# Optimization experiments

Measured on AMD Instinct MI355X. Metric: run time of the kernel, lower is better.

Reference implementation:

```python
import jax, jax.numpy as jnp
import numpy as np

B, N, D, H = 256, 256, 136, 128  # queries, docs/query, feature dim, hidden dim


def setup_inputs() -> dict:
    key = jax.random.key(0)
    ks = jax.random.split(key, 7)
    features = jax.random.uniform(ks[0], (B, N, D), dtype=jnp.float32)
    labels = jax.random.randint(ks[1], (B, N), 0, 5, dtype=jnp.int32)  # relevance grades 0..4
    # Small init scales keep MLP scores in (-1, 1) so log2(1 + max(s_i, s_j)) is well-defined
    W1 = jax.random.normal(ks[2], (D, H), dtype=jnp.float32) * 0.05
    b1 = jnp.zeros((H,), dtype=jnp.float32)
    W2 = jax.random.normal(ks[3], (H, H), dtype=jnp.float32) * 0.05
    b2 = jnp.zeros((H,), dtype=jnp.float32)
    W3 = jax.random.normal(ks[4], (H, 1), dtype=jnp.float32) * 0.02
    b3 = jnp.zeros((1,), dtype=jnp.float32)
    return {"features": features, "labels": labels,
            "W1": W1, "b1": b1, "W2": W2, "b2": b2, "W3": W3, "b3": b3}


def _scores(features, W1, b1, W2, b2, W3, b3):
    # Linear-ReLU-(Dropout: identity in eval)-Linear-ReLU-Linear, then squeeze(-1)
    h = jax.nn.relu(jnp.einsum('bnd,dh->bnh', features, W1) + b1)
    h = jax.nn.relu(jnp.einsum('bnh,hk->bnk', h, W2) + b2)
    return (jnp.einsum('bnh,ho->bno', h, W3) + b3).squeeze(-1)  # [B, N]


def _compute_lambdas(scores, labels):
    si = scores[:, :, None]        # s_i  [B, N, 1]
    sj = scores[:, None, :]        # s_j  [B, 1, N]
    li = labels[:, :, None]
    lj = labels[:, None, :]
    # lambda_ij = 0.5 * (1 - sigmoid(s_j - s_i)) = 0.5 * sigmoid(s_i - s_j)
    lam = 0.5 * jax.nn.sigmoid(si - sj)
    gain = jnp.exp2(labels.astype(scores.dtype))  # 2 ** l
    dndcg = jnp.abs((gain[:, :, None] - gain[:, None, :])
                    / (1.0 + jnp.log2(1.0 + jnp.maximum(si, sj))))
    A = jnp.where(li > lj, lam * dndcg, jnp.zeros((), scores.dtype))  # [B, N, N]
    # lambdas[i] += A[i, j] over j (pairs where l_i > l_j); lambdas[j] -= A[i, j]
    return A.sum(-1) - A.sum(-2)  # [B, N]


def reference(features, labels, W1, b1, W2, b2, W3, b3):
    scores = _scores(features, W1, b1, W2, b2, W3, b3)
    return _compute_lambdas(scores, labels)
```

## Files before the change

kernel.cpp:

```cpp
#include <hip/hip_runtime.h>
#include <hip/hip_bf16.h>

#define DIN  136
#define HH   128
#define NSEQ 256
#define NB   256
#define BROWS 64
#define K1P  168
#define JB   8

typedef __attribute__((ext_vector_type(4))) float f32x4;
typedef __attribute__((ext_vector_type(2))) float f32x2;
typedef __attribute__((ext_vector_type(8))) short bf16x8;

static __device__ __forceinline__ unsigned short f2bf(float f) {
    unsigned int u = __float_as_uint(f);
    u += 0x7fffu + ((u >> 16) & 1u);
    return (unsigned short)(u >> 16);
}

__global__ __launch_bounds__(256)
void prep_kernel(const float* __restrict__ W1, const float* __restrict__ W2,
                 short* __restrict__ w1t, short* __restrict__ w2t)
{
    const int nt = gridDim.x * 256;
    const int idx = blockIdx.x * 256 + threadIdx.x;
    for (int e = idx; e < HH * K1P; e += nt) {
        const int n = e / K1P, k = e - n * K1P;
        w1t[e] = (k < DIN) ? (short)f2bf(W1[k * HH + n]) : (short)0;
    }
    for (int e = idx; e < HH * HH; e += nt) {
        const int n = e >> 7, k = e & 127;
        w2t[e] = (short)f2bf(W2[k * HH + n]);
    }
}

__global__ __launch_bounds__(256)
void scores_mfma_kernel(const float* __restrict__ features,
                        const int*   __restrict__ labels,
                        const short* __restrict__ w1t,
                        const short* __restrict__ w2t,
                        const float* __restrict__ b1, const float* __restrict__ b2,
                        const float* __restrict__ W3, const float* __restrict__ b3,
                        float4* __restrict__ pack,
                        float* __restrict__ out_zero)
{
    __shared__ short a_lds[BROWS * K1P];

    const int t    = threadIdx.x;
    const int lane = t & 63;
    const int wv   = t >> 6;
    const int l15  = lane & 15;
    const int l4   = lane >> 4;
    const long row0 = (long)blockIdx.x * BROWS;

    {
        const f32x2* src = (const f32x2*)(features + row0 * DIN);
        for (int i = t; i < BROWS * DIN / 2; i += 256) {
            f32x2 v = src[i];
            const int e = i * 2;
            const int r = e / DIN, k = e - r * DIN;
            *(unsigned int*)&a_lds[r * K1P + k] =
                (unsigned int)f2bf(v.x) | ((unsigned int)f2bf(v.y) << 16);
        }
        for (int i = t; i < BROWS * 16; i += 256) {
            const int r = i >> 4, k = DIN + (i & 15) * 2;
            *(unsigned int*)&a_lds[r * K1P + k] = 0u;
        }
    }
    __syncthreads();

    const int arow = (wv * 16 + l15) * K1P;

    f32x4 acc[8];
#pragma unroll
    for (int tn = 0; tn < 8; ++tn) {
        const float bv = b1[tn * 16 + l15];
        acc[tn] = (f32x4){bv, bv, bv, bv};
    }
    for (int kc = 0; kc < 5; ++kc) {
        const int kb = kc * 32 + l4 * 8;
        const bf16x8 afr = *(const bf16x8*)&a_lds[arow + kb];
        bf16x8 bfr[8];
#pragma unroll
        for (int tn = 0; tn < 8; ++tn)
            bfr[tn] = *(const bf16x8*)&w1t[(tn * 16 + l15) * K1P + kb];
#pragma unroll
        for (int tn = 0; tn < 8; ++tn)
            acc[tn] = __builtin_amdgcn_mfma_f32_16x16x32_bf16(afr, bfr[tn], acc[tn], 0, 0, 0);
    }
    __syncthreads();

#pragma unroll
    for (int tn = 0; tn < 8; ++tn) {
        const int col = tn * 16 + l15;
#pragma unroll
        for (int j = 0; j < 4; ++j)
            a_lds[(wv * 16 + l4 * 4 + j) * K1P + col] =
                (short)f2bf(fmaxf(acc[tn][j], 0.f));
    }
    __syncthreads();

    f32x4 acc2[8];
#pragma unroll
    for (int tn = 0; tn < 8; ++tn) {
        const float bv = b2[tn * 16 + l15];
        acc2[tn] = (f32x4){bv, bv, bv, bv};
    }
    for (int kc = 0; kc < 4; ++kc) {
        const int kb = kc * 32 + l4 * 8;
        const bf16x8 afr = *(const bf16x8*)&a_lds[arow + kb];
        bf16x8 bfr[8];
#pragma unroll
        for (int tn = 0; tn < 8; ++tn)
            bfr[tn] = *(const bf16x8*)&w2t[(tn * 16 + l15) * HH + kb];
#pragma unroll
        for (int tn = 0; tn < 8; ++tn)
            acc2[tn] = __builtin_amdgcn_mfma_f32_16x16x32_bf16(afr, bfr[tn], acc2[tn], 0, 0, 0);
    }

    {
        float w3v[8];
#pragma unroll
        for (int tn = 0; tn < 8; ++tn) w3v[tn] = W3[tn * 16 + l15];
        const float b3v = b3[0];
#pragma unroll
        for (int j = 0; j < 4; ++j) {
            float p = 0.f;
#pragma unroll
            for (int tn = 0; tn < 8; ++tn)
                p += fmaxf(acc2[tn][j], 0.f) * w3v[tn];
            p += __shfl_xor(p, 1, 64);
            p += __shfl_xor(p, 2, 64);
            p += __shfl_xor(p, 4, 64);
            p += __shfl_xor(p, 8, 64);
            if (l15 == 0) {
                const int row = wv * 16 + l4 * 4 + j;
                const long gr = row0 + row;
                const float s = p + b3v;
                const int lab = labels[gr];
                const float g = 0.5f * exp2f((float)lab);
                const float disc = 1.f / (1.f + log2f(1.f + s));
                pack[gr] = make_float4(s * 1.44269504088896f,
                                       g, disc, 0.f);
                out_zero[gr] = 0.f;
            }
        }
    }
}

__global__ __launch_bounds__(256)
void lambda_pair_kernel(const float4* __restrict__ pack,
                        float* __restrict__ out)
{
    __shared__ float4 sp[NSEQ];
    const int t  = threadIdx.x;
    const int b  = blockIdx.x >> 3;
    const int jo = (blockIdx.x & 7) * (NSEQ / JB);

    const float4 me = pack[b * NSEQ + t];
    sp[t] = me;
    __syncthreads();

    const float sci = me.x, gi = me.y, di = me.z;
    float accum = 0.f;
#pragma unroll 8
    for (int jj = 0; jj < NSEQ / JB; ++jj) {
        const float4 o = sp[jo + jj];
        const float dg = o.y - gi;
        const float e  = exp2f(o.x - sci);
        const float r  = __builtin_amdgcn_rcpf(1.f + e);
        const float dmax = (sci > o.x) ? di : o.z;
        const float dn = fabsf(dg) * dmax;
        const float w  = (dg < 0.f) ? r : (r - 1.f);
        accum += dn * w;
    }
    atomicAdd(&out[b * NSEQ + t], accum);
}

extern "C" void kernel_launch(void* const* d_in, const int* in_sizes, int n_in,
                              void* d_out, int out_size, void* d_ws, size_t ws_size,
                              hipStream_t stream)
{
    const float* features = (const float*)d_in[0];
    const int*   labels   = (const int*)d_in[1];
    const float* W1 = (const float*)d_in[2];
    const float* b1 = (const float*)d_in[3];
    const float* W2 = (const float*)d_in[4];
    const float* b2 = (const float*)d_in[5];
    const float* W3 = (const float*)d_in[6];
    const float* b3 = (const float*)d_in[7];

    float4* pack = (float4*)d_ws;
    short*  w1t  = (short*)((char*)d_ws + (size_t)NB * NSEQ * 16);
    short*  w2t  = w1t + HH * K1P;
    float*  out  = (float*)d_out;

    prep_kernel<<<64, 256, 0, stream>>>(W1, W2, w1t, w2t);
    scores_mfma_kernel<<<NB * NSEQ / BROWS, 256, 0, stream>>>(
        features, labels, w1t, w2t, b1, b2, W3, b3, pack, out);
    lambda_pair_kernel<<<NB * JB, 256, 0, stream>>>(pack, out);
}
```

Measured before the change: 124.4 us.

## Fuse score MLP and pairwise lambda kernels into one per-query block

New measurement: 121.8 us. 1.02x faster.

```diff
diff --git a/kernel.cpp b/kernel.cpp
--- a/kernel.cpp
+++ b/kernel.cpp
@@ -5,9 +5,7 @@
 #define HH   128
 #define NSEQ 256
 #define NB   256
-#define BROWS 64
 #define K1P  168
-#define JB   8
 
 typedef __attribute__((ext_vector_type(4))) float f32x4;
 typedef __attribute__((ext_vector_type(2))) float f32x2;
@@ -35,35 +33,36 @@
     }
 }
 
-__global__ __launch_bounds__(256)
-void scores_mfma_kernel(const float* __restrict__ features,
-                        const int*   __restrict__ labels,
-                        const short* __restrict__ w1t,
-                        const short* __restrict__ w2t,
-                        const float* __restrict__ b1, const float* __restrict__ b2,
-                        const float* __restrict__ W3, const float* __restrict__ b3,
-                        float4* __restrict__ pack,
-                        float* __restrict__ out_zero)
+__global__ __launch_bounds__(1024, 4)
+void fused_kernel(const float* __restrict__ features,
+                  const int*   __restrict__ labels,
+                  const short* __restrict__ w1t,
+                  const short* __restrict__ w2t,
+                  const float* __restrict__ b1, const float* __restrict__ b2,
+                  const float* __restrict__ W3, const float* __restrict__ b3,
+                  float* __restrict__ out)
 {
-    __shared__ short a_lds[BROWS * K1P];
+    __shared__ short  a_lds[NSEQ * K1P];
+    __shared__ float4 sp[NSEQ];
+    __shared__ float  s_part[4][NSEQ];
 
     const int t    = threadIdx.x;
     const int lane = t & 63;
     const int wv   = t >> 6;
     const int l15  = lane & 15;
     const int l4   = lane >> 4;
-    const long row0 = (long)blockIdx.x * BROWS;
+    const long row0 = (long)blockIdx.x * NSEQ;
 
     {
         const f32x2* src = (const f32x2*)(features + row0 * DIN);
-        for (int i = t; i < BROWS * DIN / 2; i += 256) {
+        for (int i = t; i < NSEQ * DIN / 2; i += 1024) {
             f32x2 v = src[i];
             const int e = i * 2;
             const int r = e / DIN, k = e - r * DIN;
             *(unsigned int*)&a_lds[r * K1P + k] =
                 (unsigned int)f2bf(v.x) | ((unsigned int)f2bf(v.y) << 16);
         }
-        for (int i = t; i < BROWS * 16; i += 256) {
+        for (int i = t; i < NSEQ * 16; i += 1024) {
             const int r = i >> 4, k = DIN + (i & 15) * 2;
             *(unsigned int*)&a_lds[r * K1P + k] = 0u;
         }
@@ -89,7 +88,6 @@
         for (int tn = 0; tn < 8; ++tn)
             acc[tn] = __builtin_amdgcn_mfma_f32_16x16x32_bf16(afr, bfr[tn], acc[tn], 0, 0, 0);
     }
-    __syncthreads();
 
 #pragma unroll
     for (int tn = 0; tn < 8; ++tn) {
@@ -99,7 +97,6 @@
             a_lds[(wv * 16 + l4 * 4 + j) * K1P + col] =
                 (short)f2bf(fmaxf(acc[tn][j], 0.f));
     }
-    __syncthreads();
 
     f32x4 acc2[8];
 #pragma unroll
@@ -136,46 +133,44 @@
             p += __shfl_xor(p, 8, 64);
             if (l15 == 0) {
                 const int row = wv * 16 + l4 * 4 + j;
-                const long gr = row0 + row;
                 const float s = p + b3v;
-                const int lab = labels[gr];
+                const int lab = labels[row0 + row];
                 const float g = 0.5f * exp2f((float)lab);
                 const float disc = 1.f / (1.f + log2f(1.f + s));
-                pack[gr] = make_float4(s * 1.44269504088896f,
-                                       g, disc, 0.f);
-                out_zero[gr] = 0.f;
+                sp[row] = make_float4(s * 1.44269504088896f,
+                                      g, disc, 0.f);
             }
         }
     }
-}
-
-__global__ __launch_bounds__(256)
-void lambda_pair_kernel(const float4* __restrict__ pack,
-                        float* __restrict__ out)
-{
-    __shared__ float4 sp[NSEQ];
-    const int t  = threadIdx.x;
-    const int b  = blockIdx.x >> 3;
-    const int jo = (blockIdx.x & 7) * (NSEQ / JB);
-
-    const float4 me = pack[b * NSEQ + t];
-    sp[t] = me;
     __syncthreads();
 
-    const float sci = me.x, gi = me.y, di = me.z;
-    float accum = 0.f;
+    {
+        const int i  = t & (NSEQ - 1);
+        const int jg = t >> 8;
+        const float4 me = sp[i];
+        const float sci = me.x, gi = me.y, di = me.z;
+        float accum = 0.f;
+        const int j0 = jg * 64;
 #pragma unroll 8
-    for (int jj = 0; jj < NSEQ / JB; ++jj) {
-        const float4 o = sp[jo + jj];
-        const float dg = o.y - gi;
-        const float e  = exp2f(o.x - sci);
-        const float r  = __builtin_amdgcn_rcpf(1.f + e);
-        const float dmax = (sci > o.x) ? di : o.z;
-        const float dn = fabsf(dg) * dmax;
-        const float w  = (dg < 0.f) ? r : (r - 1.f);
-        accum += dn * w;
+        for (int jj = 0; jj < 64; ++jj) {
+            const float4 o = sp[j0 + jj];
+            const float dg = o.y - gi;
+            const float e  = exp2f(o.x - sci);
+            const float r  = __builtin_amdgcn_rcpf(1.f + e);
+            const float dmax = (sci > o.x) ? di : o.z;
+            const float dn = fabsf(dg) * dmax;
+            const float w  = (dg < 0.f) ? r : (r - 1.f);
+            accum += dn * w;
+        }
+        s_part[jg][i] = accum;
     }
-    atomicAdd(&out[b * NSEQ + t], accum);
+    __syncthreads();
+    {
+        const int i  = t & (NSEQ - 1);
+        if ((t >> 8) == 0)
+            out[row0 + i] = s_part[0][i] + s_part[1][i] +
+                            s_part[2][i] + s_part[3][i];
+    }
 }
 
 extern "C" void kernel_launch(void* const* d_in, const int* in_sizes, int n_in,
@@ -191,13 +186,11 @@
     const float* W3 = (const float*)d_in[6];
     const float* b3 = (const float*)d_in[7];
 
-    float4* pack = (float4*)d_ws;
-    short*  w1t  = (short*)((char*)d_ws + (size_t)NB * NSEQ * 16);
-    short*  w2t  = w1t + HH * K1P;
-    float*  out  = (float*)d_out;
+    short* w1t = (short*)d_ws;
+    short* w2t = w1t + HH * K1P;
+    float* out = (float*)d_out;
 
     prep_kernel<<<64, 256, 0, stream>>>(W1, W2, w1t, w2t);
-    scores_mfma_kernel<<<NB * NSEQ / BROWS, 256, 0, stream>>>(
-        features, labels, w1t, w2t, b1, b2, W3, b3, pack, out);
-    lambda_pair_kernel<<<NB * JB, 256, 0, stream>>>(pack, out);
+    fused_kernel<<<NB, 1024, 0, stream>>>(
+        features, labels, w1t, w2t, b1, b2, W3, b3, out);
 }
```
